# Kernel optimization log

Hardware: AMD Instinct MI355X
Metric: run time of the kernel (lower is better)

## Reference

```python
import jax, jax.numpy as jnp
import numpy as np

B, N_FEAT, D = 16384, 32, 64
HID1, HID2, HOF = 1024, 512, 64
OUT = 1
N_PAIRS = N_FEAT * (N_FEAT - 1) // 2
EPS = 1e-5


def setup_inputs() -> dict:
    key = jax.random.key(0)
    ks = jax.random.split(key, 16)
    s = 0.02
    return {
        "x": jax.random.normal(ks[0], (B, N_FEAT, D), dtype=jnp.float32),
        "W1": jax.random.normal(ks[1], (N_FEAT * D, HID1), dtype=jnp.float32) * s,
        "b1": jnp.zeros((HID1,), jnp.float32),
        "g1": jnp.ones((HID1,), jnp.float32),
        "beta1": jnp.zeros((HID1,), jnp.float32),
        "W2": jax.random.normal(ks[2], (HID1, HID2), dtype=jnp.float32) * s,
        "b2": jnp.zeros((HID2,), jnp.float32),
        "g2": jnp.ones((HID2,), jnp.float32),
        "beta2": jnp.zeros((HID2,), jnp.float32),
        "W3": jax.random.normal(ks[3], (HID2, HOF), dtype=jnp.float32) * s,
        "b3": jnp.zeros((HOF,), jnp.float32),
        "Wc": jax.random.normal(ks[4], (HOF + N_PAIRS, OUT), dtype=jnp.float32) * s,
        "bc": jnp.zeros((OUT,), jnp.float32),
    }


def _batchnorm(h, g, beta):
    # BatchNorm1d in training mode: batch mean / biased variance
    m = jnp.mean(h, axis=0)
    v = jnp.var(h, axis=0)
    return g * (h - m) * jax.lax.rsqrt(v + EPS) + beta


_IU, _JU = np.triu_indices(N_FEAT, k=1)  # same (i<j) order as nested loop


def reference(x, W1, b1, g1, beta1, W2, b2, g2, beta2, W3, b3, Wc, bc):
    # second-order interactions: all pairwise dot products, gathered upper-tri
    gram = jnp.einsum("bnd,bmd->bnm", x, x)          # [B, N, N]
    pairs = gram[:, _IU, _JU]                          # [B, N*(N-1)/2]
    # deep processor
    flat = x.reshape(x.shape[0], -1)                   # [B, N*D]
    h = _batchnorm(jax.nn.relu(flat @ W1 + b1), g1, beta1)
    h = _batchnorm(jax.nn.relu(h @ W2 + b2), g2, beta2)
    hof = h @ W3 + b3                                  # [B, HOF]
    inter = jnp.concatenate([hof, pairs], axis=1)
    return inter @ Wc + bc
```

## Files before the change

kernel.cpp:

```cpp
#include <hip/hip_runtime.h>
#include <stdint.h>

typedef unsigned short u16;
typedef __attribute__((ext_vector_type(8))) short short8;
typedef __attribute__((ext_vector_type(4))) float f32x4;

#define BATCH 16384L

__device__ __forceinline__ u16 f2bf(float f) {
    union { float f; uint32_t u; } cv; cv.f = f;
    uint32_t u = cv.u;
    u = (u + 0x7fffu + ((u >> 16) & 1u)) >> 16;
    return (u16)u;
}
__device__ __forceinline__ float bf2f(u16 h) {
    union { uint32_t u; float f; } cv; cv.u = ((uint32_t)h) << 16;
    return cv.f;
}

__global__ __launch_bounds__(256) void k_gram(const float* __restrict__ x,
                                              const float* __restrict__ Wc,
                                              u16* __restrict__ xb,
                                              float* __restrict__ spair) {
    const int wave = threadIdx.x >> 6;
    const int lane = threadIdx.x & 63;
    const long b = (long)blockIdx.x * 4 + wave;
    const int r16 = lane & 15, quad = lane >> 4;
    const float* xg = x + b * 2048;

    short8 hi[2][2], lo[2][2];
    for (int mt = 0; mt < 2; mt++) {
        for (int k0 = 0; k0 < 2; k0++) {
            const int row = mt * 16 + r16;
            const int kof = k0 * 32 + quad * 8;
            const float* p = xg + row * 64 + kof;
            float4 p0 = *(const float4*)p;
            float4 p1 = *(const float4*)(p + 4);
            float v[8] = {p0.x, p0.y, p0.z, p0.w, p1.x, p1.y, p1.z, p1.w};
            short8 h, l;
            for (int j = 0; j < 8; j++) {
                u16 hb = f2bf(v[j]);
                h[j] = (short)hb;
                l[j] = (short)f2bf(v[j] - bf2f(hb));
            }
            hi[mt][k0] = h; lo[mt][k0] = l;
            *(short8*)(xb + b * 2048 + row * 64 + kof) = h;
        }
    }
    f32x4 zero = {0.f, 0.f, 0.f, 0.f};
    f32x4 acc[2][2];
    for (int mt = 0; mt < 2; mt++) for (int nt = 0; nt < 2; nt++) acc[mt][nt] = zero;
    for (int k0 = 0; k0 < 2; k0++)
        for (int mt = 0; mt < 2; mt++)
            for (int nt = 0; nt < 2; nt++) {
                acc[mt][nt] = __builtin_amdgcn_mfma_f32_16x16x32_bf16(hi[mt][k0], hi[nt][k0], acc[mt][nt], 0, 0, 0);
                acc[mt][nt] = __builtin_amdgcn_mfma_f32_16x16x32_bf16(hi[mt][k0], lo[nt][k0], acc[mt][nt], 0, 0, 0);
                acc[mt][nt] = __builtin_amdgcn_mfma_f32_16x16x32_bf16(lo[mt][k0], hi[nt][k0], acc[mt][nt], 0, 0, 0);
            }
    float pacc = 0.f;
    for (int mt = 0; mt < 2; mt++)
        for (int nt = 0; nt < 2; nt++)
            for (int r = 0; r < 4; r++) {
                int row = mt * 16 + quad * 4 + r;
                int col = nt * 16 + r16;
                if (col > row) {
                    int p = 31 * row - (row * (row - 1)) / 2 + (col - row - 1);
                    pacc += acc[mt][nt][r] * Wc[64 + p];
                }
            }
    for (int off = 1; off < 64; off <<= 1) pacc += __shfl_xor(pacc, off);
    if (lane == 0) spair[b] = pacc;
}

__global__ __launch_bounds__(256) void k_transpose_bf16(const float* __restrict__ W,
                                                        const float* __restrict__ scale,
                                                        u16* __restrict__ WT,
                                                        int K, int N) {
    __shared__ float tile[32][33];
    const int nb = blockIdx.x * 32, kb = blockIdx.y * 32;
    const int tx = threadIdx.x & 31, ty = threadIdx.x >> 5;
    if (scale) {
        for (int r = ty; r < 32; r += 8)
            tile[r][tx] = scale[kb + r] * W[(long)(kb + r) * N + nb + tx];
    } else {
        for (int r = ty; r < 32; r += 8)
            tile[r][tx] = W[(long)(kb + r) * N + nb + tx];
    }
    __syncthreads();
    for (int r = ty; r < 32; r += 8) WT[(long)(nb + r) * K + kb + tx] = f2bf(tile[tx][r]);
}

__global__ __launch_bounds__(256) void gemm_bn(const u16* __restrict__ A,
                                               const u16* __restrict__ Bt,
                                               const float* __restrict__ bias,
                                               u16* __restrict__ C,
                                               float* __restrict__ sums,
                                               float* __restrict__ ssq,
                                               int N, int K, int lognb) {
    __shared__ u16 lA[128 * 64];
    __shared__ u16 lB[128 * 64];
    const int tid = threadIdx.x;
    const int lane = tid & 63, wave = tid >> 6;
    const int wm = wave >> 1, wn = wave & 1;
    const int quad = lane >> 4, r16 = lane & 15;
    const int px = r16 & 7;
    const int lid = blockIdx.x;
    const int xcd = lid & 7, t = lid >> 3;
    const int nbk = t & ((1 << lognb) - 1);
    const int mbk = (xcd << 4) + (t >> lognb);
    const long m0 = (long)mbk * 128;
    const long n0 = (long)nbk * 128;

    f32x4 zero = {0.f, 0.f, 0.f, 0.f};
    f32x4 acc[4][4];
    for (int mt = 0; mt < 4; mt++) for (int nt = 0; nt < 4; nt++) acc[mt][nt] = zero;

    for (long k0 = 0; k0 < K; k0 += 64) {
        __syncthreads();
        for (int i = 0; i < 4; i++) {
            const int c = tid + 256 * i;
            const int row = c >> 3, pos = c & 7;
            const int g = pos ^ (row & 7);
            const u16* ga = A + (m0 + row) * K + k0 + g * 8;
            const u16* gb = Bt + (n0 + row) * K + k0 + g * 8;
            __builtin_amdgcn_global_load_lds((const __attribute__((address_space(1))) void*)ga,
                                             (__attribute__((address_space(3))) void*)(&lA[c * 8]), 16, 0, 0);
            __builtin_amdgcn_global_load_lds((const __attribute__((address_space(1))) void*)gb,
                                             (__attribute__((address_space(3))) void*)(&lB[c * 8]), 16, 0, 0);
        }
        __syncthreads();
        for (int ks = 0; ks < 2; ks++) {
            short8 af[4], bfr[4];
            const int jb = ((ks << 2) + quad) ^ px;
            for (int mt = 0; mt < 4; mt++)
                af[mt] = *(const short8*)&lA[(wm * 64 + mt * 16 + r16) * 64 + jb * 8];
            for (int nt = 0; nt < 4; nt++)
                bfr[nt] = *(const short8*)&lB[(wn * 64 + nt * 16 + r16) * 64 + jb * 8];
            for (int mt = 0; mt < 4; mt++)
                for (int nt = 0; nt < 4; nt++)
                    acc[mt][nt] = __builtin_amdgcn_mfma_f32_16x16x32_bf16(af[mt], bfr[nt], acc[mt][nt], 0, 0, 0);
        }
    }

    for (int nt = 0; nt < 4; nt++) {
        const int col = (int)n0 + wn * 64 + nt * 16 + r16;
        const float bcol = bias[col];
        float s = 0.f, sq = 0.f;
        for (int mt = 0; mt < 4; mt++)
            for (int r = 0; r < 4; r++) {
                const long row = m0 + wm * 64 + mt * 16 + quad * 4 + r;
                float v = acc[mt][nt][r] + bcol;
                v = fmaxf(v, 0.f);
                C[row * N + col] = f2bf(v);
                s += v; sq += v * v;
            }
        s += __shfl_xor(s, 16);  s += __shfl_xor(s, 32);
        sq += __shfl_xor(sq, 16); sq += __shfl_xor(sq, 32);
        if (quad == 0) { atomicAdd(&sums[col], s); atomicAdd(&ssq[col], sq); }
    }
}

__global__ void k_stat(const float* __restrict__ sums, const float* __restrict__ ssq,
                       const float* __restrict__ g, const float* __restrict__ beta,
                       float* __restrict__ a, float* __restrict__ c, int n, float invB) {
    const int k = blockIdx.x * 256 + threadIdx.x;
    if (k < n) {
        const float m = sums[k] * invB;
        const float var = ssq[k] * invB - m * m;
        const float s = g[k] * rsqrtf(var + 1e-5f);
        a[k] = s; c[k] = beta[k] - s * m;
    }
}

__global__ __launch_bounds__(64) void k_b2adj(const float* __restrict__ W2,
                                              const float* __restrict__ c1,
                                              const float* __restrict__ b2,
                                              float* __restrict__ b2a) {
    const int col = blockIdx.x, lane = threadIdx.x;
    float s = 0.f;
    for (int k = lane; k < 1024; k += 64) s += c1[k] * W2[(long)k * 512 + col];
    for (int off = 1; off < 64; off <<= 1) s += __shfl_xor(s, off);
    if (lane == 0) b2a[col] = b2[col] + s;
}

__global__ void k_v(const float* __restrict__ W3, const float* __restrict__ b3,
                    const float* __restrict__ Wc, const float* __restrict__ bc,
                    float* __restrict__ v, float* __restrict__ c0) {
    const int k = blockIdx.x * 256 + threadIdx.x;
    if (k < 512) {
        float s = 0.f;
        for (int j = 0; j < 64; j++) s += W3[k * 64 + j] * Wc[j];
        v[k] = s;
    }
    if (k == 0) {
        float s = 0.f;
        for (int j = 0; j < 64; j++) s += b3[j] * Wc[j];
        *c0 = s + bc[0];
    }
}

__global__ __launch_bounds__(256) void k_final(const u16* __restrict__ h2,
                                               const float* __restrict__ a2,
                                               const float* __restrict__ c2,
                                               const float* __restrict__ v,
                                               const float* __restrict__ c0,
                                               const float* __restrict__ spair,
                                               float* __restrict__ out) {
    const int wave = threadIdx.x >> 6, lane = threadIdx.x & 63;
    const long b = (long)blockIdx.x * 4 + wave;
    const int k0 = lane * 8;
    short8 hv = *(const short8*)&h2[b * 512 + k0];
    float acc = 0.f;
    for (int j = 0; j < 8; j++) {
        const int k = k0 + j;
        const float f = bf2f((u16)hv[j]);
        acc += (a2[k] * f + c2[k]) * v[k];
    }
    for (int off = 1; off < 64; off <<= 1) acc += __shfl_xor(acc, off);
    if (lane == 0) out[b] = acc + spair[b] + c0[0];
}

extern "C" void kernel_launch(void* const* d_in, const int* in_sizes, int n_in,
                              void* d_out, int out_size, void* d_ws, size_t ws_size,
                              hipStream_t stream) {
    const float* x     = (const float*)d_in[0];
    const float* W1    = (const float*)d_in[1];
    const float* b1    = (const float*)d_in[2];
    const float* g1    = (const float*)d_in[3];
    const float* beta1 = (const float*)d_in[4];
    const float* W2    = (const float*)d_in[5];
    const float* b2    = (const float*)d_in[6];
    const float* g2    = (const float*)d_in[7];
    const float* beta2 = (const float*)d_in[8];
    const float* W3    = (const float*)d_in[9];
    const float* b3    = (const float*)d_in[10];
    const float* Wc    = (const float*)d_in[11];
    const float* bc    = (const float*)d_in[12];
    float* out = (float*)d_out;

    char* ws = (char*)d_ws;
    size_t o = 0;
    u16* xb  = (u16*)(ws + o); o += BATCH * 2048 * 2;
    u16* w1t = (u16*)(ws + o); o += 2048L * 1024 * 2;
    u16* w2t = (u16*)(ws + o); o += 1024L * 512 * 2;
    u16* h1b = (u16*)(ws + o); o += BATCH * 1024 * 2;
    u16* h2b = (u16*)(ws + o); o += BATCH * 512 * 2;
    float* spair = (float*)(ws + o); o += BATCH * 4;
    float* stats = (float*)(ws + o); o += 3072 * 4;
    float* sums1 = stats, *ssq1 = stats + 1024, *sums2 = stats + 2048, *ssq2 = stats + 2560;
    float* a1 = (float*)(ws + o); o += 1024 * 4;
    float* c1 = (float*)(ws + o); o += 1024 * 4;
    float* a2 = (float*)(ws + o); o += 512 * 4;
    float* c2 = (float*)(ws + o); o += 512 * 4;
    float* vv = (float*)(ws + o); o += 512 * 4;
    float* c0 = (float*)(ws + o); o += 4;
    float* b2a = (float*)(ws + o); o += 512 * 4;

    hipMemsetAsync(stats, 0, 3072 * 4, stream);
    k_gram<<<4096, 256, 0, stream>>>(x, Wc, xb, spair);
    k_transpose_bf16<<<dim3(1024 / 32, 2048 / 32), 256, 0, stream>>>(W1, nullptr, w1t, 2048, 1024);
    gemm_bn<<<1024, 256, 0, stream>>>(xb, w1t, b1, h1b, sums1, ssq1, 1024, 2048, 3);
    k_stat<<<4, 256, 0, stream>>>(sums1, ssq1, g1, beta1, a1, c1, 1024, 1.f / 16384.f);
    k_transpose_bf16<<<dim3(512 / 32, 1024 / 32), 256, 0, stream>>>(W2, a1, w2t, 1024, 512);
    k_b2adj<<<512, 64, 0, stream>>>(W2, c1, b2, b2a);
    gemm_bn<<<512, 256, 0, stream>>>(h1b, w2t, b2a, h2b, sums2, ssq2, 512, 1024, 2);
    k_stat<<<2, 256, 0, stream>>>(sums2, ssq2, g2, beta2, a2, c2, 512, 1.f / 16384.f);
    k_v<<<2, 256, 0, stream>>>(W3, b3, Wc, bc, vv, c0);
    k_final<<<4096, 256, 0, stream>>>(h2b, a2, c2, vv, c0, spair, out);
}
```

Before: 365.9 us.

## Switch deep-MLP GEMMs and intermediates from bf16 to fp8 with weight scaling

Stores x, the transposed weights and the hidden activations as fp8 (e4m3) instead of bf16, and runs both GEMMs with fp8 MFMA at a K-step of 128. Weights are scaled by 64 before quantisation and the accumulator is rescaled in the epilogue. This halves memory traffic for activations and weights and doubles MFMA throughput per instruction. In exchange it loses a lot of precision, which risks exceeding the accuracy tolerance, particularly for the BN-normalised outputs.

Result: faster. 336.6 us (-8.0%).

```diff
diff --git a/kernel.cpp b/kernel.cpp
--- a/kernel.cpp
+++ b/kernel.cpp
@@ -2,10 +2,13 @@
 #include <stdint.h>
 
 typedef unsigned short u16;
+typedef unsigned char u8;
 typedef __attribute__((ext_vector_type(8))) short short8;
 typedef __attribute__((ext_vector_type(4))) float f32x4;
 
 #define BATCH 16384L
+#define WSCALE 64.0f
+#define INV_WSCALE (1.0f / 64.0f)
 
 __device__ __forceinline__ u16 f2bf(float f) {
     union { float f; uint32_t u; } cv; cv.f = f;
@@ -17,10 +20,17 @@
     union { uint32_t u; float f; } cv; cv.u = ((uint32_t)h) << 16;
     return cv.f;
 }
+template<bool HI>
+__device__ __forceinline__ uint32_t fp8pk(float a, float b, uint32_t old) {
+    return (uint32_t)__builtin_amdgcn_cvt_pk_fp8_f32(a, b, (int)old, HI);
+}
+__device__ __forceinline__ u8 f2fp8(float v) {
+    return (u8)(__builtin_amdgcn_cvt_pk_fp8_f32(v, v, 0, false) & 0xff);
+}
 
 __global__ __launch_bounds__(256) void k_gram(const float* __restrict__ x,
                                               const float* __restrict__ Wc,
-                                              u16* __restrict__ xb,
+                                              u8* __restrict__ xb,
                                               float* __restrict__ spair) {
     const int wave = threadIdx.x >> 6;
     const int lane = threadIdx.x & 63;
@@ -44,7 +54,9 @@
                 l[j] = (short)f2bf(v[j] - bf2f(hb));
             }
             hi[mt][k0] = h; lo[mt][k0] = l;
-            *(short8*)(xb + b * 2048 + row * 64 + kof) = h;
+            uint32_t w0 = fp8pk<false>(v[0], v[1], 0); w0 = fp8pk<true>(v[2], v[3], w0);
+            uint32_t w1 = fp8pk<false>(v[4], v[5], 0); w1 = fp8pk<true>(v[6], v[7], w1);
+            *(uint2*)(xb + b * 2048 + row * 64 + kof) = make_uint2(w0, w1);
         }
     }
     f32x4 zero = {0.f, 0.f, 0.f, 0.f};
@@ -72,10 +84,10 @@
     if (lane == 0) spair[b] = pacc;
 }
 
-__global__ __launch_bounds__(256) void k_transpose_bf16(const float* __restrict__ W,
-                                                        const float* __restrict__ scale,
-                                                        u16* __restrict__ WT,
-                                                        int K, int N) {
+__global__ __launch_bounds__(256) void k_transpose_fp8(const float* __restrict__ W,
+                                                       const float* __restrict__ scale,
+                                                       u8* __restrict__ WT,
+                                                       int K, int N) {
     __shared__ float tile[32][33];
     const int nb = blockIdx.x * 32, kb = blockIdx.y * 32;
     const int tx = threadIdx.x & 31, ty = threadIdx.x >> 5;
@@ -87,27 +99,28 @@
             tile[r][tx] = W[(long)(kb + r) * N + nb + tx];
     }
     __syncthreads();
-    for (int r = ty; r < 32; r += 8) WT[(long)(nb + r) * K + kb + tx] = f2bf(tile[tx][r]);
-}
-
-__global__ __launch_bounds__(256) void gemm_bn(const u16* __restrict__ A,
-                                               const u16* __restrict__ Bt,
+    for (int r = ty; r < 32; r += 8)
+        WT[(long)(nb + r) * K + kb + tx] = f2fp8(WSCALE * tile[tx][r]);
+}
+
+template<int LOGNB>
+__global__ __launch_bounds__(256) void gemm_bn(const u8* __restrict__ A,
+                                               const u8* __restrict__ Bt,
                                                const float* __restrict__ bias,
-                                               u16* __restrict__ C,
+                                               u8* __restrict__ C,
                                                float* __restrict__ sums,
                                                float* __restrict__ ssq,
-                                               int N, int K, int lognb) {
-    __shared__ u16 lA[128 * 64];
-    __shared__ u16 lB[128 * 64];
+                                               int N, int K, float inv) {
+    __shared__ u8 lA[128 * 128];
+    __shared__ u8 lB[128 * 128];
     const int tid = threadIdx.x;
     const int lane = tid & 63, wave = tid >> 6;
     const int wm = wave >> 1, wn = wave & 1;
     const int quad = lane >> 4, r16 = lane & 15;
-    const int px = r16 & 7;
     const int lid = blockIdx.x;
     const int xcd = lid & 7, t = lid >> 3;
-    const int nbk = t & ((1 << lognb) - 1);
-    const int mbk = (xcd << 4) + (t >> lognb);
+    const int nbk = t & ((1 << LOGNB) - 1);
+    const int mbk = (xcd << 4) + (t >> LOGNB);
     const long m0 = (long)mbk * 128;
     const long n0 = (long)nbk * 128;
 
@@ -115,30 +128,36 @@
     f32x4 acc[4][4];
     for (int mt = 0; mt < 4; mt++) for (int nt = 0; nt < 4; nt++) acc[mt][nt] = zero;
 
-    for (long k0 = 0; k0 < K; k0 += 64) {
+    const int gcb = quad >> 1, off8 = (quad & 1) * 8;
+
+    for (long k0 = 0; k0 < K; k0 += 128) {
         __syncthreads();
         for (int i = 0; i < 4; i++) {
             const int c = tid + 256 * i;
             const int row = c >> 3, pos = c & 7;
             const int g = pos ^ (row & 7);
-            const u16* ga = A + (m0 + row) * K + k0 + g * 8;
-            const u16* gb = Bt + (n0 + row) * K + k0 + g * 8;
+            const u8* ga = A + (m0 + row) * K + k0 + g * 16;
+            const u8* gb = Bt + (n0 + row) * K + k0 + g * 16;
             __builtin_amdgcn_global_load_lds((const __attribute__((address_space(1))) void*)ga,
-                                             (__attribute__((address_space(3))) void*)(&lA[c * 8]), 16, 0, 0);
+                                             (__attribute__((address_space(3))) void*)(&lA[c * 16]), 16, 0, 0);
             __builtin_amdgcn_global_load_lds((const __attribute__((address_space(1))) void*)gb,
-                                             (__attribute__((address_space(3))) void*)(&lB[c * 8]), 16, 0, 0);
+                                             (__attribute__((address_space(3))) void*)(&lB[c * 16]), 16, 0, 0);
         }
         __syncthreads();
-        for (int ks = 0; ks < 2; ks++) {
-            short8 af[4], bfr[4];
-            const int jb = ((ks << 2) + quad) ^ px;
-            for (int mt = 0; mt < 4; mt++)
-                af[mt] = *(const short8*)&lA[(wm * 64 + mt * 16 + r16) * 64 + jb * 8];
-            for (int nt = 0; nt < 4; nt++)
-                bfr[nt] = *(const short8*)&lB[(wn * 64 + nt * 16 + r16) * 64 + jb * 8];
+        for (int ks = 0; ks < 4; ks++) {
+            const int gc = ks * 2 + gcb;
+            long af[4], bfr[4];
+            for (int mt = 0; mt < 4; mt++) {
+                const int R = wm * 64 + mt * 16 + r16;
+                af[mt] = *(const long*)&lA[R * 128 + ((gc ^ (R & 7)) * 16) + off8];
+            }
+            for (int nt = 0; nt < 4; nt++) {
+                const int R = wn * 64 + nt * 16 + r16;
+                bfr[nt] = *(const long*)&lB[R * 128 + ((gc ^ (R & 7)) * 16) + off8];
+            }
             for (int mt = 0; mt < 4; mt++)
                 for (int nt = 0; nt < 4; nt++)
-                    acc[mt][nt] = __builtin_amdgcn_mfma_f32_16x16x32_bf16(af[mt], bfr[nt], acc[mt][nt], 0, 0, 0);
+                    acc[mt][nt] = __builtin_amdgcn_mfma_f32_16x16x32_fp8_fp8(af[mt], bfr[nt], acc[mt][nt], 0, 0, 0);
         }
     }
 
@@ -149,9 +168,9 @@
         for (int mt = 0; mt < 4; mt++)
             for (int r = 0; r < 4; r++) {
                 const long row = m0 + wm * 64 + mt * 16 + quad * 4 + r;
-                float v = acc[mt][nt][r] + bcol;
+                float v = acc[mt][nt][r] * inv + bcol;
                 v = fmaxf(v, 0.f);
-                C[row * N + col] = f2bf(v);
+                C[row * N + col] = f2fp8(v);
                 s += v; sq += v * v;
             }
         s += __shfl_xor(s, 16);  s += __shfl_xor(s, 32);
@@ -199,7 +218,7 @@
     }
 }
 
-__global__ __launch_bounds__(256) void k_final(const u16* __restrict__ h2,
+__global__ __launch_bounds__(256) void k_final(const u8* __restrict__ h2,
                                                const float* __restrict__ a2,
                                                const float* __restrict__ c2,
                                                const float* __restrict__ v,
@@ -209,12 +228,20 @@
     const int wave = threadIdx.x >> 6, lane = threadIdx.x & 63;
     const long b = (long)blockIdx.x * 4 + wave;
     const int k0 = lane * 8;
-    short8 hv = *(const short8*)&h2[b * 512 + k0];
+    uint2 hv = *(const uint2*)&h2[b * 512 + k0];
+    float f[8];
+    f[0] = __builtin_amdgcn_cvt_f32_fp8(hv.x, 0);
+    f[1] = __builtin_amdgcn_cvt_f32_fp8(hv.x, 1);
+    f[2] = __builtin_amdgcn_cvt_f32_fp8(hv.x, 2);
+    f[3] = __builtin_amdgcn_cvt_f32_fp8(hv.x, 3);
+    f[4] = __builtin_amdgcn_cvt_f32_fp8(hv.y, 0);
+    f[5] = __builtin_amdgcn_cvt_f32_fp8(hv.y, 1);
+    f[6] = __builtin_amdgcn_cvt_f32_fp8(hv.y, 2);
+    f[7] = __builtin_amdgcn_cvt_f32_fp8(hv.y, 3);
     float acc = 0.f;
     for (int j = 0; j < 8; j++) {
         const int k = k0 + j;
-        const float f = bf2f((u16)hv[j]);
-        acc += (a2[k] * f + c2[k]) * v[k];
+        acc += (a2[k] * f[j] + c2[k]) * v[k];
     }
     for (int off = 1; off < 64; off <<= 1) acc += __shfl_xor(acc, off);
     if (lane == 0) out[b] = acc + spair[b] + c0[0];
@@ -240,11 +267,11 @@
 
     char* ws = (char*)d_ws;
     size_t o = 0;
-    u16* xb  = (u16*)(ws + o); o += BATCH * 2048 * 2;
-    u16* w1t = (u16*)(ws + o); o += 2048L * 1024 * 2;
-    u16* w2t = (u16*)(ws + o); o += 1024L * 512 * 2;
-    u16* h1b = (u16*)(ws + o); o += BATCH * 1024 * 2;
-    u16* h2b = (u16*)(ws + o); o += BATCH * 512 * 2;
+    u8* xb  = (u8*)(ws + o); o += BATCH * 2048;
+    u8* w1f = (u8*)(ws + o); o += 2048L * 1024;
+    u8* w2f = (u8*)(ws + o); o += 1024L * 512;
+    u8* h1b = (u8*)(ws + o); o += BATCH * 1024;
+    u8* h2b = (u8*)(ws + o); o += BATCH * 512;
     float* spair = (float*)(ws + o); o += BATCH * 4;
     float* stats = (float*)(ws + o); o += 3072 * 4;
     float* sums1 = stats, *ssq1 = stats + 1024, *sums2 = stats + 2048, *ssq2 = stats + 2560;
@@ -256,14 +283,14 @@
     float* c0 = (float*)(ws + o); o += 4;
     float* b2a = (float*)(ws + o); o += 512 * 4;
 
-    hipMemsetAsync(stats, 0, 3072 * 4, stream);
+    (void)hipMemsetAsync(stats, 0, 3072 * 4, stream);
     k_gram<<<4096, 256, 0, stream>>>(x, Wc, xb, spair);
-    k_transpose_bf16<<<dim3(1024 / 32, 2048 / 32), 256, 0, stream>>>(W1, nullptr, w1t, 2048, 1024);
-    gemm_bn<<<1024, 256, 0, stream>>>(xb, w1t, b1, h1b, sums1, ssq1, 1024, 2048, 3);
+    k_transpose_fp8<<<dim3(1024 / 32, 2048 / 32), 256, 0, stream>>>(W1, nullptr, w1f, 2048, 1024);
+    gemm_bn<3><<<1024, 256, 0, stream>>>(xb, w1f, b1, h1b, sums1, ssq1, 1024, 2048, INV_WSCALE);
     k_stat<<<4, 256, 0, stream>>>(sums1, ssq1, g1, beta1, a1, c1, 1024, 1.f / 16384.f);
-    k_transpose_bf16<<<dim3(512 / 32, 1024 / 32), 256, 0, stream>>>(W2, a1, w2t, 1024, 512);
+    k_transpose_fp8<<<dim3(512 / 32, 1024 / 32), 256, 0, stream>>>(W2, a1, w2f, 1024, 512);
     k_b2adj<<<512, 64, 0, stream>>>(W2, c1, b2, b2a);
-    gemm_bn<<<512, 256, 0, stream>>>(h1b, w2t, b2a, h2b, sums2, ssq2, 512, 1024, 2);
+    gemm_bn<2><<<512, 256, 0, stream>>>(h1b, w2f, b2a, h2b, sums2, ssq2, 512, 1024, INV_WSCALE);
     k_stat<<<2, 256, 0, stream>>>(sums2, ssq2, g2, beta2, a2, c2, 512, 1.f / 16384.f);
     k_v<<<2, 256, 0, stream>>>(W3, b3, Wc, bc, vv, c0);
     k_final<<<4096, 256, 0, stream>>>(h2b, a2, c2, vv, c0, spair, out);
```
